# Kernel tuning notes

Measured on AMD Instinct MI355X. Metric: run time of the kernel, lower is better.

The kernel has to match this reference:

```python
import jax, jax.numpy as jnp
import numpy as np

B, N, D_IN = 2, 2048, 2048
D_OUT, H, KV = 2048, 32, 8
G = H // KV          # group_size = 4
DH = D_OUT // H      # head dim = 64


def setup_inputs() -> dict:
    key = jax.random.key(0)
    k0, k1, k2, k3, k4, k5 = jax.random.split(key, 6)
    s_in = 1.0 / np.sqrt(D_IN)
    s_out = 1.0 / np.sqrt(D_OUT)
    return {
        "x": jax.random.normal(k0, (B, N, D_IN), dtype=jnp.float32),
        "Wq": jax.random.normal(k1, (D_IN, H * DH), dtype=jnp.float32) * s_in,
        "Wk": jax.random.normal(k2, (D_IN, KV * DH), dtype=jnp.float32) * s_in,
        "Wv": jax.random.normal(k3, (D_IN, KV * DH), dtype=jnp.float32) * s_in,
        "Wo": jax.random.normal(k4, (D_OUT, D_IN), dtype=jnp.float32) * s_out,
        "bo": jax.random.normal(k5, (D_IN,), dtype=jnp.float32) * 0.01,
    }


def gqa_forward(x, Wq, Wk, Wv, Wo, bo):
    b, n, _ = x.shape
    scale = 1.0 / jnp.sqrt(jnp.asarray(DH, x.dtype))
    # projections
    q = (x @ Wq).reshape(b, n, KV, G, DH)   # queries grouped by shared kv head
    k = (x @ Wk).reshape(b, n, KV, DH)
    v = (x @ Wv).reshape(b, n, KV, DH)
    # scores: (B, KV, G, N, N) — equivalent to repeat_interleave of K over groups
    scores = jnp.einsum('bnkgd,bmkd->bkgnm', q, k) * scale
    causal = jnp.triu(jnp.ones((n, n), dtype=bool), k=1)
    scores = jnp.where(causal, -jnp.inf, scores)
    attn = jax.nn.softmax(scores, axis=-1)
    # dropout p=0.0 -> identity
    ctx = jnp.einsum('bkgnm,bmkd->bnkgd', attn, v).reshape(b, n, D_OUT)
    return ctx @ Wo + bo


def reference(x, Wq, Wk, Wv, Wo, bo):
    return gqa_forward(x, Wq, Wk, Wv, Wo, bo)
```

## Files before the change

### kernel.cpp

```cpp
#include <hip/hip_runtime.h>
#include <hip/hip_bf16.h>
#include <cstdint>


#define B_    2
#define N_    2048
#define DIN_  2048
#define H_    32
#define KV_   8
#define DH_   64
#define M_    4096
#define NQKV_ 3072

typedef float f32x4 __attribute__((ext_vector_type(4)));
typedef __bf16 bf16x8 __attribute__((ext_vector_type(8)));
typedef unsigned short u16x8 __attribute__((ext_vector_type(8)));

__device__ __forceinline__ unsigned short f32_to_bf16_bits(float f) {
  unsigned int u = __float_as_uint(f);
  u = (u + 0x7FFFu + ((u >> 16) & 1u)) >> 16;
  return (unsigned short)u;
}

__device__ __forceinline__ void gload_lds16(const void* g, void* l) {
  __builtin_amdgcn_global_load_lds(
      (__attribute__((address_space(1))) void*)(g),
      (__attribute__((address_space(3))) void*)(l), 16, 0, 0);
}

__global__ __launch_bounds__(256) void prep(
    const float* __restrict__ x, const float* __restrict__ Wq,
    const float* __restrict__ Wk, const float* __restrict__ Wv,
    const float* __restrict__ Wo,
    unsigned short* __restrict__ Xb, unsigned short* __restrict__ Wqkv,
    unsigned short* __restrict__ Wot, float qscale) {
  const int task = blockIdx.y, tid = threadIdx.x;
  if (task == 0) {
    size_t i0 = ((size_t)blockIdx.x * 256 + tid) * 2;
#pragma unroll
    for (int t = 0; t < 2; ++t) {
      float4 v = ((const float4*)x)[i0 + t];
      ushort4 o;
      o.x = f32_to_bf16_bits(v.x);
      o.y = f32_to_bf16_bits(v.y);
      o.z = f32_to_bf16_bits(v.z);
      o.w = f32_to_bf16_bits(v.w);
      ((ushort4*)Xb)[i0 + t] = o;
    }
    return;
  }
  const float* src;
  unsigned short* dst;
  int NC, off;
  float scale = 1.0f;
  switch (task) {
    case 1: src = Wq; dst = Wqkv; NC = 2048; off = 0;    scale = qscale; break;
    case 2: src = Wk; dst = Wqkv; NC = 512;  off = 2048; break;
    case 3: src = Wv; dst = Wqkv; NC = 512;  off = 2560; break;
    default: src = Wo; dst = Wot; NC = 2048; off = 0;    break;
  }
  const int nx = NC >> 5;
  const int bx = blockIdx.x;
  if (bx >= nx * 64) return;
  const int n0 = (bx % nx) * 32, k0 = (bx / nx) * 32;
  __shared__ float tile[32][33];
  const int tx = tid & 31, ty = tid >> 5;
#pragma unroll
  for (int i = 0; i < 32; i += 8)
    tile[ty + i][tx] = src[(size_t)(k0 + ty + i) * NC + n0 + tx];
  __syncthreads();
#pragma unroll
  for (int i = 0; i < 32; i += 8)
    dst[(size_t)(off + n0 + ty + i) * 2048 + k0 + tx] =
        f32_to_bf16_bits(tile[tx][ty + i] * scale);
}

__global__ __launch_bounds__(256) void transpose_v(
    const unsigned short* __restrict__ QKV, unsigned short* __restrict__ Vtg) {
  __shared__ unsigned short t[64][72];
  int nt = blockIdx.x, bkv = blockIdx.y;
  int b = bkv >> 3, kv = bkv & 7;
  int tid = threadIdx.x;
  int row = tid >> 2, c = (tid & 3) * 16;
  const unsigned short* src =
      QKV + (size_t)(b * N_ + nt * 64 + row) * NQKV_ + 2560 + kv * 64;
  *(u16x8*)&t[row][c]     = *(const u16x8*)(src + c);
  *(u16x8*)&t[row][c + 8] = *(const u16x8*)(src + c + 8);
  __syncthreads();
  int d = tid >> 2;
  unsigned short* dst = Vtg + ((size_t)bkv * 64 + d) * N_ + nt * 64 + c;
  u16x8 o0, o1;
#pragma unroll
  for (int i = 0; i < 8; ++i) { o0[i] = t[c + i][d]; o1[i] = t[c + 8 + i][d]; }
  *(u16x8*)dst = o0;
  *(u16x8*)(dst + 8) = o1;
}

template <bool OUT_BF16, bool BIAS>
__global__ __launch_bounds__(512, 2) void gemm256(
    const unsigned short* __restrict__ A,
    const unsigned short* __restrict__ Bt,
    void* __restrict__ Cv,
    const float* __restrict__ bias,
    int Nn, int K, int nbx) {
  __shared__ unsigned short lds[4][2][8192];

  const int tid = threadIdx.x;
  const int lane = tid & 63;
  const int wave = tid >> 6;
  const int wm = wave >> 2, wn = wave & 3;
  const int l16 = lane & 15, quad = lane >> 4;

  const int nwg = gridDim.x;
  const int orig = blockIdx.x;
  const int bid = (orig & 7) * (nwg >> 3) + (orig >> 3);
  const int m0 = (bid / nbx) * 256, n0 = (bid % nbx) * 256;

  const int T = K >> 5;

  auto stage = [&](int t, int part, const unsigned short* src, int r0) {
    unsigned short* db = &lds[t & 3][part][0];
#pragma unroll
    for (int c = 0; c < 2; ++c) {
      int off = c * 8192 + tid * 16;
      int row = off >> 6;
      int kch = ((off >> 4) & 3) ^ ((row >> 1) & 3);
      gload_lds16(src + (size_t)(r0 + row) * K + t * 32 + kch * 8,
                  (char*)db + off);
    }
  };

  f32x4 acc[8][4] = {};

#pragma unroll
  for (int t = 0; t < 3; ++t) {
    stage(t, 0, A, m0);
    stage(t, 1, Bt, n0);
  }

  for (int t = 0; t < T; ++t) {
    if (t + 2 < T)      asm volatile("s_waitcnt vmcnt(8)" ::: "memory");
    else if (t + 1 < T) asm volatile("s_waitcnt vmcnt(4)" ::: "memory");
    else                asm volatile("s_waitcnt vmcnt(0)" ::: "memory");
    __builtin_amdgcn_s_barrier();
    asm volatile("" ::: "memory");

    const char* Ab = (const char*)&lds[t & 3][0][0];
    const char* Bb = (const char*)&lds[t & 3][1][0];

    bf16x8 a[4], b[4];
#pragma unroll
    for (int mi = 0; mi < 4; ++mi) {
      int row = wm * 128 + mi * 16 + l16;
      a[mi] = *(const bf16x8*)(Ab + row * 64 + (quad ^ ((row >> 1) & 3)) * 16);
    }
#pragma unroll
    for (int ni = 0; ni < 4; ++ni) {
      int row = wn * 64 + ni * 16 + l16;
      b[ni] = *(const bf16x8*)(Bb + row * 64 + (quad ^ ((row >> 1) & 3)) * 16);
    }
    if (t + 3 < T) stage(t + 3, 0, A, m0);
    asm volatile("" ::: "memory");
    __builtin_amdgcn_s_barrier();
    asm volatile("s_waitcnt lgkmcnt(0)" ::: "memory");
    __builtin_amdgcn_s_setprio(1);
#pragma unroll
    for (int mi = 0; mi < 4; ++mi)
#pragma unroll
      for (int ni = 0; ni < 4; ++ni)
        acc[mi][ni] = __builtin_amdgcn_mfma_f32_16x16x32_bf16(
            a[mi], b[ni], acc[mi][ni], 0, 0, 0);
    __builtin_amdgcn_s_setprio(0);
    asm volatile("" ::: "memory");
    __builtin_amdgcn_s_barrier();
    asm volatile("" ::: "memory");

    bf16x8 a2[4];
#pragma unroll
    for (int mi = 0; mi < 4; ++mi) {
      int row = wm * 128 + 64 + mi * 16 + l16;
      a2[mi] = *(const bf16x8*)(Ab + row * 64 + (quad ^ ((row >> 1) & 3)) * 16);
    }
    if (t + 3 < T) stage(t + 3, 1, Bt, n0);
    asm volatile("" ::: "memory");
    __builtin_amdgcn_s_barrier();
    asm volatile("s_waitcnt lgkmcnt(0)" ::: "memory");
    __builtin_amdgcn_s_setprio(1);
#pragma unroll
    for (int mi = 0; mi < 4; ++mi)
#pragma unroll
      for (int ni = 0; ni < 4; ++ni)
        acc[mi + 4][ni] = __builtin_amdgcn_mfma_f32_16x16x32_bf16(
            a2[mi], b[ni], acc[mi + 4][ni], 0, 0, 0);
    __builtin_amdgcn_s_setprio(0);
  }

  unsigned short* Cb = (unsigned short*)Cv;
  float* Cf = (float*)Cv;
#pragma unroll
  for (int mi = 0; mi < 8; ++mi) {
    int rrow = m0 + wm * 128 + mi * 16 + quad * 4;
#pragma unroll
    for (int ni = 0; ni < 4; ++ni) {
      int col = n0 + wn * 64 + ni * 16 + l16;
      float bv = BIAS ? bias[col] : 0.0f;
#pragma unroll
      for (int r = 0; r < 4; ++r) {
        float v = acc[mi][ni][r] + bv;
        if (OUT_BF16)
          Cb[(size_t)(rrow + r) * Nn + col] = f32_to_bf16_bits(v);
        else
          Cf[(size_t)(rrow + r) * Nn + col] = v;
      }
    }
  }
}

__global__ __launch_bounds__(256, 2) void attn_fwd(
    const unsigned short* __restrict__ QKV,
    const unsigned short* __restrict__ Vtg,
    unsigned short* __restrict__ Ctx) {
  __shared__ unsigned short Ks[2][64 * 64];
  __shared__ unsigned short Vs[2][64 * 64];
  __shared__ unsigned short Ps[2][4][2][16 * 64];

  const int p = blockIdx.x;
  const int kv = blockIdx.y >> 1, hp = blockIdx.y & 1;
  const int b = blockIdx.z;
  const int tid = threadIdx.x, lane = tid & 63, wave = tid >> 6;
  const int l16 = lane & 15, quad = lane >> 4;
  const int h = kv * 4 + hp * 2 + (wave >> 1);
  const int rhalf = (wave & 1) * 32;
  const size_t baserow = (size_t)b * N_;
  const unsigned short* Kg = QKV + 2048 + kv * 64;
  const unsigned short* Vg = Vtg + (size_t)(b * KV_ + kv) * 64 * N_;
  const unsigned short* Qbase = QKV + baserow * NQKV_ + h * 64;
  const int sw = l16 & 7;

  auto stageKV = [&](int j, int buf) {
#pragma unroll
    for (int it = 0; it < 2; ++it) {
      int c = tid + it * 256;
      int row = c >> 3, off = ((c & 7) ^ (row & 7)) * 8;
      gload_lds16(Kg + (baserow + j * 64 + row) * NQKV_ + off,
                  (char*)Ks[buf] + c * 16);
      gload_lds16(Vg + (size_t)row * N_ + j * 64 + off,
                  (char*)Vs[buf] + c * 16);
    }
  };

#pragma unroll 1
  for (int phase = 0; phase < 2; ++phase) {
    const int qtile = phase ? p : 31 - p;
    const int q0 = qtile * 64;

    bf16x8 qa[2][2];
#pragma unroll
    for (int s = 0; s < 2; ++s)
#pragma unroll
      for (int ks = 0; ks < 2; ++ks)
        qa[s][ks] = *(const bf16x8*)(Qbase +
            (size_t)(q0 + rhalf + s * 16 + l16) * NQKV_ + ks * 32 + quad * 8);

    f32x4 oacc[2][4] = {};
    float lp[2][4] = {};

    __syncthreads();
    stageKV(0, 0);

    for (int j = 0; j <= qtile; ++j) {
      __syncthreads();
      const int buf = j & 1;
      if (j < qtile) stageKV(j + 1, buf ^ 1);

      bf16x8 kb[2][4];
#pragma unroll
      for (int ks = 0; ks < 2; ++ks)
#pragma unroll
        for (int ni = 0; ni < 4; ++ni)
          kb[ks][ni] = *(const bf16x8*)&Ks[buf][(ni * 16 + l16) * 64 +
                                               ((ks * 4 + quad) ^ sw) * 8];

#pragma unroll
      for (int s = 0; s < 2; ++s) {
        f32x4 sc[4] = {};
        __builtin_amdgcn_s_setprio(1);
#pragma unroll
        for (int ks = 0; ks < 2; ++ks)
#pragma unroll
          for (int ni = 0; ni < 4; ++ni)
            sc[ni] = __builtin_amdgcn_mfma_f32_16x16x32_bf16(
                qa[s][ks], kb[ks][ni], sc[ni], 0, 0, 0);
        __builtin_amdgcn_s_setprio(0);
        if (j == qtile) {
          const int qrow = q0 + rhalf + s * 16 + quad * 4;
#pragma unroll
          for (int ni = 0; ni < 4; ++ni) {
            int kcol = q0 + ni * 16 + l16;
#pragma unroll
            for (int r = 0; r < 4; ++r)
              if (kcol > qrow + r) sc[ni][r] = -1e30f;
          }
        }
        unsigned short* Pw = &Ps[buf][wave][s][0];
#pragma unroll
        for (int ni = 0; ni < 4; ++ni) {
          const int cl = ni * 2 + (l16 >> 3);
#pragma unroll
          for (int r = 0; r < 4; ++r) {
            float pe = __builtin_amdgcn_exp2f(sc[ni][r]);
            lp[s][r] += pe;
            int row = quad * 4 + r;
            Pw[row * 64 + ((cl ^ (row & 7)) * 8) + (l16 & 7)] =
                (unsigned short)(__float_as_uint(pe) >> 16);
          }
        }
      }

      bf16x8 vb[2][4];
#pragma unroll
      for (int ks = 0; ks < 2; ++ks)
#pragma unroll
        for (int di = 0; di < 4; ++di)
          vb[ks][di] = *(const bf16x8*)&Vs[buf][(di * 16 + l16) * 64 +
                                               ((ks * 4 + quad) ^ sw) * 8];
#pragma unroll
      for (int s = 0; s < 2; ++s) {
        bf16x8 pa[2];
#pragma unroll
        for (int ks = 0; ks < 2; ++ks)
          pa[ks] = *(const bf16x8*)&Ps[buf][wave][s][l16 * 64 +
                                                    ((ks * 4 + quad) ^ sw) * 8];
        __builtin_amdgcn_s_setprio(1);
#pragma unroll
        for (int ks = 0; ks < 2; ++ks)
#pragma unroll
          for (int di = 0; di < 4; ++di)
            oacc[s][di] = __builtin_amdgcn_mfma_f32_16x16x32_bf16(
                pa[ks], vb[ks][di], oacc[s][di], 0, 0, 0);
        __builtin_amdgcn_s_setprio(0);
      }
    }

#pragma unroll
    for (int s = 0; s < 2; ++s) {
      float inv[4];
#pragma unroll
      for (int r = 0; r < 4; ++r) {
        float v = lp[s][r];
#pragma unroll
        for (int off = 1; off < 16; off <<= 1) v += __shfl_xor(v, off);
        inv[r] = 1.0f / v;
      }
#pragma unroll
      for (int di = 0; di < 4; ++di)
#pragma unroll
        for (int r = 0; r < 4; ++r) {
          size_t row = baserow + q0 + rhalf + s * 16 + quad * 4 + r;
          Ctx[row * 2048 + h * 64 + di * 16 + l16] =
              f32_to_bf16_bits(oacc[s][di][r] * inv[r]);
        }
    }
  }
}

extern "C" void kernel_launch(void* const* d_in, const int* in_sizes, int n_in,
                              void* d_out, int out_size, void* d_ws, size_t ws_size,
                              hipStream_t stream) {
  const float* x  = (const float*)d_in[0];
  const float* Wq = (const float*)d_in[1];
  const float* Wk = (const float*)d_in[2];
  const float* Wv = (const float*)d_in[3];
  const float* Wo = (const float*)d_in[4];
  const float* bo = (const float*)d_in[5];
  float* out = (float*)d_out;

  unsigned short* Xb   = (unsigned short*)d_ws;
  unsigned short* Wqkv = Xb + (size_t)M_ * DIN_;
  unsigned short* QKV  = Wqkv + (size_t)NQKV_ * DIN_;
  unsigned short* Wot  = QKV + (size_t)M_ * NQKV_;
  unsigned short* Ctx  = Xb;
  unsigned short* Vtg  = Wqkv;

  const float kQScale = 0.125f * 1.44269504088896340736f;

  prep<<<dim3(4096, 5), 256, 0, stream>>>(x, Wq, Wk, Wv, Wo, Xb, Wqkv, Wot, kQScale);

  gemm256<true, false><<<dim3(192), 512, 0, stream>>>(
      Xb, Wqkv, QKV, nullptr, NQKV_, DIN_, NQKV_ / 256);

  transpose_v<<<dim3(N_ / 64, B_ * KV_), 256, 0, stream>>>(QKV, Vtg);

  attn_fwd<<<dim3(16, 16, 2), 256, 0, stream>>>(QKV, Vtg, Ctx);

  gemm256<false, true><<<dim3(128), 512, 0, stream>>>(
      Ctx, Wot, out, bo, DIN_, 2048, DIN_ / 256);
}
```

Measured before the change: 303.5 us.

## Restructure GEMM mainloop to K=64 double-buffered stages with intra-tile A prefetch

The 256x256 GEMM now loads K=64 slices into two LDS buffers instead of four K=32 buffers, with an 8-way XOR swizzle sized for the 128-byte rows. Inside each slice, A fragments are software-pipelined: the next pair of M sub-tiles is read from LDS while MFMAs run on the current pair, and sched_barriers pin the instruction order. The goal is fewer barriers per K step and better overlap of LDS reads with MFMA. In exchange the pipeline is shallower (prefetch distance 2 instead of 3), so global-load latency is hidden less, and register pressure rises.

Result: no change. 302.6 us (-0.3%).

```diff
diff --git a/kernel.cpp b/kernel.cpp
--- a/kernel.cpp
+++ b/kernel.cpp
@@ -97,13 +97,13 @@
 }
 
 template <bool OUT_BF16, bool BIAS>
-__global__ __launch_bounds__(512, 2) void gemm256(
+__global__ __launch_bounds__(512, 2) void gemm256p(
     const unsigned short* __restrict__ A,
     const unsigned short* __restrict__ Bt,
     void* __restrict__ Cv,
     const float* __restrict__ bias,
     int Nn, int K, int nbx) {
-  __shared__ unsigned short lds[4][2][8192];
+  __shared__ unsigned short lds[2][2][16384];
 
   const int tid = threadIdx.x;
   const int lane = tid & 63;
@@ -116,83 +116,92 @@
   const int bid = (orig & 7) * (nwg >> 3) + (orig >> 3);
   const int m0 = (bid / nbx) * 256, n0 = (bid % nbx) * 256;
 
-  const int T = K >> 5;
-
-  auto stage = [&](int t, int part, const unsigned short* src, int r0) {
-    unsigned short* db = &lds[t & 3][part][0];
-#pragma unroll
-    for (int c = 0; c < 2; ++c) {
-      int off = c * 8192 + tid * 16;
-      int row = off >> 6;
-      int kch = ((off >> 4) & 3) ^ ((row >> 1) & 3);
-      gload_lds16(src + (size_t)(r0 + row) * K + t * 32 + kch * 8,
-                  (char*)db + off);
+  const int T = K >> 6;
+
+  auto stage = [&](int c) {
+    const int buf = c & 1;
+#pragma unroll
+    for (int part = 0; part < 2; ++part) {
+      const unsigned short* src = part ? Bt : A;
+      const int r0 = part ? n0 : m0;
+#pragma unroll
+      for (int i = 0; i < 4; ++i) {
+        int off = i * 8192 + tid * 16;
+        int row = off >> 7;
+        int kch = ((off >> 4) & 7) ^ (row & 7);
+        gload_lds16(src + (size_t)(r0 + row) * K + c * 64 + kch * 8,
+                    (char*)&lds[buf][part][0] + off);
+      }
     }
   };
 
+  const int sw7 = l16 & 7;
+  const int cA0 = ((0 * 4 + quad) ^ sw7) * 16;
+  const int cA1 = ((1 * 4 + quad) ^ sw7) * 16;
+  const int rowA = (wm * 128 + l16) * 128;
+  const int rowB = (wn * 64 + l16) * 128;
+
   f32x4 acc[8][4] = {};
 
-#pragma unroll
-  for (int t = 0; t < 3; ++t) {
-    stage(t, 0, A, m0);
-    stage(t, 1, Bt, n0);
-  }
-
-  for (int t = 0; t < T; ++t) {
-    if (t + 2 < T)      asm volatile("s_waitcnt vmcnt(8)" ::: "memory");
-    else if (t + 1 < T) asm volatile("s_waitcnt vmcnt(4)" ::: "memory");
-    else                asm volatile("s_waitcnt vmcnt(0)" ::: "memory");
+  stage(0);
+  stage(1);
+
+  for (int c = 0; c < T; ++c) {
+    if (c + 1 < T) asm volatile("s_waitcnt vmcnt(8)" ::: "memory");
+    else           asm volatile("s_waitcnt vmcnt(0)" ::: "memory");
     __builtin_amdgcn_s_barrier();
     asm volatile("" ::: "memory");
 
-    const char* Ab = (const char*)&lds[t & 3][0][0];
-    const char* Bb = (const char*)&lds[t & 3][1][0];
-
-    bf16x8 a[4], b[4];
-#pragma unroll
-    for (int mi = 0; mi < 4; ++mi) {
-      int row = wm * 128 + mi * 16 + l16;
-      a[mi] = *(const bf16x8*)(Ab + row * 64 + (quad ^ ((row >> 1) & 3)) * 16);
-    }
+    const char* Ar = (const char*)&lds[c & 1][0][0];
+    const char* Br = (const char*)&lds[c & 1][1][0];
+
+    bf16x8 b[4][2];
 #pragma unroll
     for (int ni = 0; ni < 4; ++ni) {
-      int row = wn * 64 + ni * 16 + l16;
-      b[ni] = *(const bf16x8*)(Bb + row * 64 + (quad ^ ((row >> 1) & 3)) * 16);
-    }
-    if (t + 3 < T) stage(t + 3, 0, A, m0);
-    asm volatile("" ::: "memory");
-    __builtin_amdgcn_s_barrier();
+      b[ni][0] = *(const bf16x8*)(Br + rowB + ni * 2048 + cA0);
+      b[ni][1] = *(const bf16x8*)(Br + rowB + ni * 2048 + cA1);
+    }
+    bf16x8 ap[2][2][2];
+#pragma unroll
+    for (int ml = 0; ml < 2; ++ml) {
+      ap[0][ml][0] = *(const bf16x8*)(Ar + rowA + ml * 2048 + cA0);
+      ap[0][ml][1] = *(const bf16x8*)(Ar + rowA + ml * 2048 + cA1);
+    }
     asm volatile("s_waitcnt lgkmcnt(0)" ::: "memory");
-    __builtin_amdgcn_s_setprio(1);
-#pragma unroll
-    for (int mi = 0; mi < 4; ++mi)
-#pragma unroll
-      for (int ni = 0; ni < 4; ++ni)
-        acc[mi][ni] = __builtin_amdgcn_mfma_f32_16x16x32_bf16(
-            a[mi], b[ni], acc[mi][ni], 0, 0, 0);
-    __builtin_amdgcn_s_setprio(0);
+    __builtin_amdgcn_sched_barrier(0);
+
+#pragma unroll
+    for (int p = 0; p < 4; ++p) {
+      if (p < 3) {
+        const int nx = (p + 1) & 1;
+#pragma unroll
+        for (int ml = 0; ml < 2; ++ml) {
+          int mi = (p + 1) * 2 + ml;
+          ap[nx][ml][0] = *(const bf16x8*)(Ar + rowA + mi * 2048 + cA0);
+          ap[nx][ml][1] = *(const bf16x8*)(Ar + rowA + mi * 2048 + cA1);
+        }
+      }
+      __builtin_amdgcn_sched_barrier(0);
+      __builtin_amdgcn_s_setprio(1);
+#pragma unroll
+      for (int ml = 0; ml < 2; ++ml)
+#pragma unroll
+        for (int ni = 0; ni < 4; ++ni)
+#pragma unroll
+          for (int ks = 0; ks < 2; ++ks)
+            acc[p * 2 + ml][ni] = __builtin_amdgcn_mfma_f32_16x16x32_bf16(
+                ap[p & 1][ml][ks], b[ni][ks], acc[p * 2 + ml][ni], 0, 0, 0);
+      __builtin_amdgcn_s_setprio(0);
+      if (p < 3) {
+        asm volatile("s_waitcnt lgkmcnt(0)" ::: "memory");
+        __builtin_amdgcn_sched_barrier(0);
+      }
+    }
+
     asm volatile("" ::: "memory");
     __builtin_amdgcn_s_barrier();
     asm volatile("" ::: "memory");
-
-    bf16x8 a2[4];
-#pragma unroll
-    for (int mi = 0; mi < 4; ++mi) {
-      int row = wm * 128 + 64 + mi * 16 + l16;
-      a2[mi] = *(const bf16x8*)(Ab + row * 64 + (quad ^ ((row >> 1) & 3)) * 16);
-    }
-    if (t + 3 < T) stage(t + 3, 1, Bt, n0);
-    asm volatile("" ::: "memory");
-    __builtin_amdgcn_s_barrier();
-    asm volatile("s_waitcnt lgkmcnt(0)" ::: "memory");
-    __builtin_amdgcn_s_setprio(1);
-#pragma unroll
-    for (int mi = 0; mi < 4; ++mi)
-#pragma unroll
-      for (int ni = 0; ni < 4; ++ni)
-        acc[mi + 4][ni] = __builtin_amdgcn_mfma_f32_16x16x32_bf16(
-            a2[mi], b[ni], acc[mi + 4][ni], 0, 0, 0);
-    __builtin_amdgcn_s_setprio(0);
+    if (c + 2 < T) stage(c + 2);
   }
 
   unsigned short* Cb = (unsigned short*)Cv;
@@ -386,13 +395,13 @@
 
   prep<<<dim3(4096, 5), 256, 0, stream>>>(x, Wq, Wk, Wv, Wo, Xb, Wqkv, Wot, kQScale);
 
-  gemm256<true, false><<<dim3(192), 512, 0, stream>>>(
+  gemm256p<true, false><<<dim3(192), 512, 0, stream>>>(
       Xb, Wqkv, QKV, nullptr, NQKV_, DIN_, NQKV_ / 256);
 
   transpose_v<<<dim3(N_ / 64, B_ * KV_), 256, 0, stream>>>(QKV, Vtg);
 
   attn_fwd<<<dim3(16, 16, 2), 256, 0, stream>>>(QKV, Vtg, Ctx);
 
-  gemm256<false, true><<<dim3(128), 512, 0, stream>>>(
+  gemm256p<false, true><<<dim3(128), 512, 0, stream>>>(
       Ctx, Wot, out, bo, DIN_, 2048, DIN_ / 256);
 }
```
